# Kernel optimization log

Measured on AMD Instinct MI355X. Metric: run time of the kernel, lower is better.

The kernel has to match this reference:

```python
import jax, jax.numpy as jnp
import numpy as np

B, C, H, W, K = 16, 384, 48, 48, 3
PAD = K // 2


def _conv1x1(x, Wt, b):
    # torch Conv2d 1x1: out[b,o,h,w] = sum_i W[o,i]*x[b,i,h,w] + b[o]
    return jnp.einsum('oi,bihw->bohw', Wt, x) + b[None, :, None, None]


def setup_inputs() -> dict:
    key = jax.random.key(0)
    ks = jax.random.split(key, 11)
    s = 0.02  # small init scale for weights
    return {
        'x': jax.random.normal(ks[0], (B, C, H, W), jnp.float32),
        'Wq': jax.random.normal(ks[1], (C, C), jnp.float32) * s,
        'bq': jnp.zeros((C,), jnp.float32),
        'Wk': jax.random.normal(ks[2], (C, C), jnp.float32) * s,
        'bk': jnp.zeros((C,), jnp.float32),
        'Wv': jax.random.normal(ks[3], (C, C), jnp.float32) * s,
        'bv': jnp.zeros((C,), jnp.float32),
        'Wg': jax.random.normal(ks[4], (K * K, K * K), jnp.float32) * s,
        'bg': jnp.zeros((K * K,), jnp.float32),
        'Wp': jax.random.normal(ks[5], (C, C), jnp.float32) * s,
        'bp': jnp.zeros((C,), jnp.float32),
    }


def reference(x, Wq, bq, Wk, bk, Wv, bv, Wg, bg, Wp, bp):
    # v_proj
    value = _conv1x1(x, Wv, bv)  # [B,C,H,W]

    # _generate_kernels: q_proj -> adaptive avg pool to (K,K) -> linear(9->9)
    qk = _conv1x1(x, Wq, bq)
    # H,W divisible by K => adaptive pool == mean over equal blocks
    qk = qk.reshape(B, C, K, H // K, K, W // K).mean(axis=(3, 5))  # [B,C,K,K]
    qk = qk.reshape(B, C, K * K)
    kernels = jnp.einsum('bcp,qp->bcq', qk, Wg) + bg  # nn.Linear: x @ W.T + b
    kernels = kernels.reshape(B, C, K, K)

    # k = k_proj(global avg pool(x))  -> [B,C,1,1]
    emb = x.mean(axis=(2, 3))  # [B,C]
    k = jnp.einsum('oi,bi->bo', Wk, emb) + bk  # [B,C]

    # residual modification of kernels
    mean_per_kernel = kernels.mean(axis=(2, 3), keepdims=True)  # [B,C,1,1]
    factor = jax.nn.sigmoid(k)[:, :, None, None]
    kernels = kernels - factor * mean_per_kernel  # [B,C,K,K]

    # dynamic per-sample per-channel depthwise conv (cross-correlation, 'same' pad)
    xp = jnp.pad(value, ((0, 0), (0, 0), (PAD, PAD), (PAD, PAD)))
    # patches[b,c,p,h,w] = value[b,c,h+i-PAD,w+j-PAD], p = i*K+j
    patches = jnp.stack(
        [xp[:, :, i:i + H, j:j + W] for i in range(K) for j in range(K)], axis=2
    )  # [B,C,K*K,H,W]
    out = jnp.einsum('bcphw,bcp->bchw', patches, kernels.reshape(B, C, K * K))

    return _conv1x1(out, Wp, bp)
```

## Files before the change

### kernel.cpp

```cpp
#include <hip/hip_runtime.h>
#include <cstdint>
#include <cstddef>

#define B_  16
#define C_  384
#define H_  48
#define W_  48
#define HW_ 2304

typedef __bf16 bf16x8 __attribute__((ext_vector_type(8)));
typedef float  f32x4  __attribute__((ext_vector_type(4)));
typedef unsigned short u16x8 __attribute__((ext_vector_type(8)));

typedef __attribute__((address_space(3))) void       lds_void;
typedef const __attribute__((address_space(1))) void gbl_void;

__device__ __forceinline__ unsigned short f2bf(float f) {
    union { float f; unsigned int u; } v; v.f = f;
    unsigned int r = v.u + 0x7fffu + ((v.u >> 16) & 1u);
    return (unsigned short)(r >> 16);
}
__device__ __forceinline__ float bf2f(unsigned short u) {
    union { unsigned int u; float f; } v; v.u = ((unsigned int)u) << 16;
    return v.f;
}

__global__ void castw2_kernel(const float* __restrict__ wv, unsigned short* __restrict__ dv,
                              const float* __restrict__ wp, unsigned short* __restrict__ dp) {
    const int blk = blockIdx.x;
    const float* s = (blk < 144) ? wv : wp;
    unsigned short* d = (blk < 144) ? dv : dp;
    const int i = ((blk < 144 ? blk : blk - 144) * 256 + threadIdx.x) * 4;
    const float4 v = *(const float4*)&s[i];
    ushort4 o; o.x = f2bf(v.x); o.y = f2bf(v.y); o.z = f2bf(v.z); o.w = f2bf(v.w);
    *(ushort4*)&d[i] = o;
}

__global__ __launch_bounds__(256) void tcast_kernel(const float* __restrict__ x,
                                                    unsigned short* __restrict__ xT) {
    __shared__ unsigned short tile[64][68];
    const int t  = threadIdx.x;
    const int b  = blockIdx.z;
    const int p0 = blockIdx.x * 64, c0 = blockIdx.y * 64;
    const float* xb = x + ((size_t)b * C_ + c0) * HW_ + p0;

#pragma unroll
    for (int pass = 0; pass < 4; ++pass) {
        const int cr = pass * 16 + (t >> 4);
        const int pc = (t & 15) * 4;
        const float4 v = *(const float4*)&xb[(size_t)cr * HW_ + pc];
        tile[pc + 0][cr] = f2bf(v.x); tile[pc + 1][cr] = f2bf(v.y);
        tile[pc + 2][cr] = f2bf(v.z); tile[pc + 3][cr] = f2bf(v.w);
    }
    __syncthreads();
    unsigned short* xTb = xT + ((size_t)b * HW_ + p0) * C_ + c0;
#pragma unroll
    for (int pass = 0; pass < 4; ++pass) {
        const int pr = pass * 16 + (t >> 4);
        const int cc = (t & 15) * 4;
        *(ushort4*)&xTb[(size_t)pr * C_ + cc] = *(const ushort4*)&tile[pr][cc];
    }
}

__global__ __launch_bounds__(256) void poolT_kernel(const unsigned short* __restrict__ xT,
                                                    float* __restrict__ px) {
    const int r  = blockIdx.x;
    const int c0 = blockIdx.y * 64;
    const int b  = blockIdx.z;
    const int t  = threadIdx.x;
    const int wv = t >> 6;
    const int l  = t & 63;
    const int i  = l >> 3;
    const int cg = l & 7;
    const int ri = r / 3, rj = r % 3;
    const int cbase = c0 + cg * 8;

    __shared__ float s[4][64];

    float acc[8] = {};
#pragma unroll
    for (int k = 0; k < 8; ++k) {
        const int pix = wv * 64 + i + k * 8;
        const int h = ri * 16 + (pix >> 4), w = rj * 16 + (pix & 15);
        const u16x8 v = *(const u16x8*)&xT[((size_t)b * HW_ + h * W_ + w) * C_ + cbase];
#pragma unroll
        for (int e = 0; e < 8; ++e) acc[e] += bf2f(v[e]);
    }
#pragma unroll
    for (int m = 8; m <= 32; m <<= 1)
#pragma unroll
        for (int e = 0; e < 8; ++e) acc[e] += __shfl_xor(acc[e], m, 64);
    if (i == 0)
#pragma unroll
        for (int e = 0; e < 8; ++e) s[wv][cg * 8 + e] = acc[e];
    __syncthreads();
    if (t < 64) {
        const float tot = s[0][t] + s[1][t] + s[2][t] + s[3][t];
        px[((size_t)b * C_ + c0 + t) * 9 + r] = tot * (1.f / 256.f);
    }
}

__global__ void small_kernel(const float* __restrict__ px,
                             const float* __restrict__ Wq, const float* __restrict__ bq,
                             const float* __restrict__ Wk, const float* __restrict__ bk,
                             const float* __restrict__ Wg, const float* __restrict__ bg,
                             unsigned short* __restrict__ kernT) {
    const int b = blockIdx.y;
    const int o = blockIdx.x * 128 + threadIdx.x;

    __shared__ float px_l[C_ * 9];
    __shared__ float emb_l[C_];
    __shared__ float wg_l[81];
    __shared__ float bg_l[9];

    for (int idx = threadIdx.x; idx < C_ * 9; idx += 128) px_l[idx] = px[(size_t)b * C_ * 9 + idx];
    if (threadIdx.x < 81) wg_l[threadIdx.x] = Wg[threadIdx.x];
    if (threadIdx.x < 9)  bg_l[threadIdx.x] = bg[threadIdx.x];
    __syncthreads();
    for (int idx = threadIdx.x; idx < C_; idx += 128) {
        float s0 = 0.f;
#pragma unroll
        for (int p = 0; p < 9; ++p) s0 += px_l[idx * 9 + p];
        emb_l[idx] = s0 * (1.f / 9.f);
    }
    __syncthreads();

    float accq[9];
#pragma unroll
    for (int p = 0; p < 9; ++p) accq[p] = bq[o];
    float acck = bk[o];
    const float* wq_row = Wq + (size_t)o * C_;
    const float* wk_row = Wk + (size_t)o * C_;
    for (int i = 0; i < C_; ++i) {
        const float w = wq_row[i];
#pragma unroll
        for (int p = 0; p < 9; ++p) accq[p] = fmaf(w, px_l[i * 9 + p], accq[p]);
        acck = fmaf(wk_row[i], emb_l[i], acck);
    }

    float kf[9], mean = 0.f;
#pragma unroll
    for (int q = 0; q < 9; ++q) {
        float a = bg_l[q];
#pragma unroll
        for (int p = 0; p < 9; ++p) a = fmaf(accq[p], wg_l[q * 9 + p], a);
        kf[q] = a; mean += a;
    }
    mean *= (1.f / 9.f);
    const float sig = 1.f / (1.f + expf(-acck));
#pragma unroll
    for (int q = 0; q < 9; ++q)
        kernT[((size_t)b * 9 + q) * C_ + o] = f2bf(kf[q] - sig * mean);
}

template<int BIAS_COL, bool OUT_BF16, int BMAJOR>
__global__ __launch_bounds__(256) void gemm_bt(const unsigned short* __restrict__ A,
                                               const unsigned short* __restrict__ Bt,
                                               const float* __restrict__ bias,
                                               void* __restrict__ Yv,
                                               int N, int nMt, int nNt, int perB,
                                               long long sA, long long sB, long long sY) {
    const int q8  = gridDim.x >> 3;
    const int swz = (blockIdx.x & 7) * q8 + (blockIdx.x >> 3);
    const int b   = swz / perB;
    const int r   = swz % perB;
    const int mtile = BMAJOR ? (r % nMt) : (r / nNt);
    const int ntile = BMAJOR ? (r / nMt) : (r % nNt);
    const int m0 = mtile * 128, n0 = ntile * 128;

    const int t = threadIdx.x;
    const int l = t & 63, w = t >> 6;
    const unsigned short* Ab = A + (size_t)b * sA;
    const unsigned short* Bb = Bt + (size_t)b * sB;

    __shared__ __align__(16) unsigned short As[128 * 64];
    __shared__ __align__(16) unsigned short Bs[128 * 64];

    f32x4 acc[4][4] = {};
    const int wm = w >> 1, wn = w & 1;

    const int srow = t >> 3;
    const int skc  = t & 7;
    const int gkc  = skc ^ (srow & 7);

    const int lr = l & 15;
    const int kq = l >> 4;
    const int xorv = lr & 7;

    for (int k0 = 0; k0 < 384; k0 += 64) {
#pragma unroll
        for (int j = 0; j < 4; ++j)
            __builtin_amdgcn_global_load_lds(
                (gbl_void*)(Ab + (size_t)(m0 + 32 * j + srow) * 384 + k0 + gkc * 8),
                (lds_void*)(As + (32 * j + srow) * 64 + skc * 8), 16, 0, 0);
#pragma unroll
        for (int j = 0; j < 4; ++j)
            __builtin_amdgcn_global_load_lds(
                (gbl_void*)(Bb + (size_t)(n0 + 32 * j + srow) * 384 + k0 + gkc * 8),
                (lds_void*)(Bs + (32 * j + srow) * 64 + skc * 8), 16, 0, 0);
        __syncthreads();

#pragma unroll
        for (int sub = 0; sub < 2; ++sub) {
            const int kc = sub * 4 + kq;
            const int ko = (kc ^ xorv) * 8;
            bf16x8 af[4], bfr[4];
#pragma unroll
            for (int f = 0; f < 4; ++f)
                af[f] = *reinterpret_cast<const bf16x8*>(&As[(wm * 64 + f * 16 + lr) * 64 + ko]);
#pragma unroll
            for (int f = 0; f < 4; ++f)
                bfr[f] = *reinterpret_cast<const bf16x8*>(&Bs[(wn * 64 + f * 16 + lr) * 64 + ko]);
#pragma unroll
            for (int fm = 0; fm < 4; ++fm)
#pragma unroll
                for (int fn = 0; fn < 4; ++fn)
                    acc[fm][fn] = __builtin_amdgcn_mfma_f32_16x16x32_bf16(af[fm], bfr[fn], acc[fm][fn], 0, 0, 0);
        }
        __syncthreads();
    }

    const int lg = (l >> 4) * 4;
#pragma unroll
    for (int fm = 0; fm < 4; ++fm) {
        const int row = m0 + wm * 64 + fm * 16 + lg;
#pragma unroll
        for (int fn = 0; fn < 4; ++fn) {
            const int col = n0 + wn * 64 + fn * 16 + lr;
            const float cb = BIAS_COL ? bias[col] : 0.f;
#pragma unroll
            for (int rr = 0; rr < 4; ++rr) {
                const float v = acc[fm][fn][rr] + (BIAS_COL ? cb : bias[row + rr]);
                if (OUT_BF16)
                    ((unsigned short*)Yv)[(size_t)b * sY + (size_t)(row + rr) * N + col] = f2bf(v);
                else
                    ((float*)Yv)[(size_t)b * sY + (size_t)(row + rr) * N + col] = v;
            }
        }
    }
}

__global__ __launch_bounds__(256) void dwT_kernel(const unsigned short* __restrict__ vT,
                                                  const unsigned short* __restrict__ kT,
                                                  unsigned short* __restrict__ oT) {
    int u = blockIdx.x * 256 + threadIdx.x;
    const int cg = u % 48;  u /= 48;
    const int p  = u % HW_;
    const int b  = u / HW_;
    const int h = p / W_, w = p % W_;
    const int c0 = cg * 8;
    const size_t base = (size_t)b * HW_ * C_;

    u16x8 kv[9];
#pragma unroll
    for (int q = 0; q < 9; ++q)
        kv[q] = *(const u16x8*)&kT[((size_t)b * 9 + q) * C_ + c0];

    float acc[8] = {};
#pragma unroll
    for (int di = 0; di < 3; ++di) {
        const int hh = h + di - 1;
        if (hh < 0 || hh >= H_) continue;
#pragma unroll
        for (int dj = 0; dj < 3; ++dj) {
            const int wn = w + dj - 1;
            if (wn < 0 || wn >= W_) continue;
            const u16x8 v = *(const u16x8*)&vT[base + (size_t)(hh * W_ + wn) * C_ + c0];
            const int q = di * 3 + dj;
#pragma unroll
            for (int e = 0; e < 8; ++e)
                acc[e] = fmaf(bf2f(v[e]), bf2f(kv[q][e]), acc[e]);
        }
    }
    u16x8 o;
#pragma unroll
    for (int e = 0; e < 8; ++e) o[e] = f2bf(acc[e]);
    *(u16x8*)&oT[base + (size_t)p * C_ + c0] = o;
}

extern "C" void kernel_launch(void* const* d_in, const int* in_sizes, int n_in,
                              void* d_out, int out_size, void* d_ws, size_t ws_size,
                              hipStream_t stream) {
    const float* x  = (const float*)d_in[0];
    const float* Wq = (const float*)d_in[1];
    const float* bq = (const float*)d_in[2];
    const float* Wk = (const float*)d_in[3];
    const float* bk = (const float*)d_in[4];
    const float* Wv = (const float*)d_in[5];
    const float* bv = (const float*)d_in[6];
    const float* Wg = (const float*)d_in[7];
    const float* bg = (const float*)d_in[8];
    const float* Wp = (const float*)d_in[9];
    const float* bp = (const float*)d_in[10];
    float* out = (float*)d_out;

    char* ws = (char*)d_ws;
    const size_t bhwc2 = (size_t)B_ * HW_ * C_ * 2;
    unsigned short* xT     = (unsigned short*)ws;
    unsigned short* valueT = (unsigned short*)(ws + bhwc2);
    unsigned short* Wvb    = (unsigned short*)(ws + 2 * bhwc2);
    unsigned short* Wpb    = (unsigned short*)(ws + 2 * bhwc2 + 294912);
    float*          px     = (float*)(ws + 2 * bhwc2 + 2 * 294912);
    unsigned short* kernT  = (unsigned short*)(ws + 2 * bhwc2 + 2 * 294912 + 221184);
    unsigned short* out2T  = xT;

    castw2_kernel<<<288, 256, 0, stream>>>(Wv, Wvb, Wp, Wpb);
    tcast_kernel<<<dim3(HW_ / 64, C_ / 64, B_), 256, 0, stream>>>(x, xT);
    poolT_kernel<<<dim3(9, C_ / 64, B_), 256, 0, stream>>>(xT, px);
    small_kernel<<<dim3(3, B_), 128, 0, stream>>>(px, Wq, bq, Wk, bk, Wg, bg, kernT);

    gemm_bt<1, true, 0><<<864, 256, 0, stream>>>(
        xT, Wvb, bv, (void*)valueT, C_, 288, 3, 864, 0LL, 0LL, 0LL);

    dwT_kernel<<<dim3((B_ * HW_ * (C_ / 8)) / 256), 256, 0, stream>>>(valueT, kernT, out2T);

    gemm_bt<0, false, 1><<<864, 256, 0, stream>>>(
        Wpb, out2T, bp, (void*)out, HW_, 3, 18, 54,
        0LL, (long long)HW_ * C_, (long long)C_ * HW_);
}
```

Baseline: 125.5 us.

## Double-buffer GEMM LDS tiles with BK=32 and 2D grid for depthwise kernel

The GEMM main loop now uses two LDS buffers of 128x32 tiles and prefetches the next K slice while running MFMAs on the current one. This removes one barrier per iteration and hides global-to-LDS latency. It adds a new XOR swizzle for the 32-wide rows and raises MFMA wave priority during compute. The depthwise kernel moves the batch index into blockIdx.y, which removes an integer divide and modulo per thread.

Measured after the change: 132.6 us. 1.06x slower.

```diff
diff --git a/kernel.cpp b/kernel.cpp
--- a/kernel.cpp
+++ b/kernel.cpp
@@ -173,52 +173,73 @@
     const unsigned short* Ab = A + (size_t)b * sA;
     const unsigned short* Bb = Bt + (size_t)b * sB;
 
-    __shared__ __align__(16) unsigned short As[128 * 64];
-    __shared__ __align__(16) unsigned short Bs[128 * 64];
+    __shared__ __align__(16) unsigned short As[2][128 * 32];
+    __shared__ __align__(16) unsigned short Bs[2][128 * 32];
 
     f32x4 acc[4][4] = {};
     const int wm = w >> 1, wn = w & 1;
 
-    const int srow = t >> 3;
-    const int skc  = t & 7;
-    const int gkc  = skc ^ (srow & 7);
+    const int srow0 = t >> 2;
+    const int sc    = t & 3;
 
     const int lr = l & 15;
     const int kq = l >> 4;
-    const int xorv = lr & 7;
-
-    for (int k0 = 0; k0 < 384; k0 += 64) {
-#pragma unroll
-        for (int j = 0; j < 4; ++j)
-            __builtin_amdgcn_global_load_lds(
-                (gbl_void*)(Ab + (size_t)(m0 + 32 * j + srow) * 384 + k0 + gkc * 8),
-                (lds_void*)(As + (32 * j + srow) * 64 + skc * 8), 16, 0, 0);
-#pragma unroll
-        for (int j = 0; j < 4; ++j)
-            __builtin_amdgcn_global_load_lds(
-                (gbl_void*)(Bb + (size_t)(n0 + 32 * j + srow) * 384 + k0 + gkc * 8),
-                (lds_void*)(Bs + (32 * j + srow) * 64 + skc * 8), 16, 0, 0);
+
+#define STAGE(BUF, K0)                                                          \
+    {                                                                           \
+        _Pragma("unroll")                                                       \
+        for (int j = 0; j < 2; ++j) {                                           \
+            const int rw = 64 * j + srow0;                                      \
+            const int gk = (sc ^ ((rw >> 1) & 3)) * 8;                          \
+            __builtin_amdgcn_global_load_lds(                                   \
+                (gbl_void*)(Ab + (size_t)(m0 + rw) * 384 + (K0) + gk),          \
+                (lds_void*)(&As[BUF][0] + rw * 32 + sc * 8), 16, 0, 0);         \
+        }                                                                       \
+        _Pragma("unroll")                                                       \
+        for (int j = 0; j < 2; ++j) {                                           \
+            const int rw = 64 * j + srow0;                                      \
+            const int gk = (sc ^ ((rw >> 1) & 3)) * 8;                          \
+            __builtin_amdgcn_global_load_lds(                                   \
+                (gbl_void*)(Bb + (size_t)(n0 + rw) * 384 + (K0) + gk),          \
+                (lds_void*)(&Bs[BUF][0] + rw * 32 + sc * 8), 16, 0, 0);         \
+        }                                                                       \
+    }
+
+    STAGE(0, 0);
+    __syncthreads();
+
+    int cur = 0;
+#pragma unroll 1
+    for (int step = 0; step < 12; ++step) {
+        if (step < 11) STAGE(cur ^ 1, (step + 1) * 32);
+
+        const unsigned short* Ac = &As[cur][0];
+        const unsigned short* Bc = &Bs[cur][0];
+        bf16x8 af[4], bfr[4];
+#pragma unroll
+        for (int f = 0; f < 4; ++f) {
+            const int row = wm * 64 + f * 16 + lr;
+            const int ko  = (kq ^ ((row >> 1) & 3)) * 8;
+            af[f] = *reinterpret_cast<const bf16x8*>(&Ac[row * 32 + ko]);
+        }
+#pragma unroll
+        for (int f = 0; f < 4; ++f) {
+            const int row = wn * 64 + f * 16 + lr;
+            const int ko  = (kq ^ ((row >> 1) & 3)) * 8;
+            bfr[f] = *reinterpret_cast<const bf16x8*>(&Bc[row * 32 + ko]);
+        }
+        __builtin_amdgcn_s_setprio(1);
+#pragma unroll
+        for (int fm = 0; fm < 4; ++fm)
+#pragma unroll
+            for (int fn = 0; fn < 4; ++fn)
+                acc[fm][fn] = __builtin_amdgcn_mfma_f32_16x16x32_bf16(af[fm], bfr[fn], acc[fm][fn], 0, 0, 0);
+        __builtin_amdgcn_s_setprio(0);
+
         __syncthreads();
-
-#pragma unroll
-        for (int sub = 0; sub < 2; ++sub) {
-            const int kc = sub * 4 + kq;
-            const int ko = (kc ^ xorv) * 8;
-            bf16x8 af[4], bfr[4];
-#pragma unroll
-            for (int f = 0; f < 4; ++f)
-                af[f] = *reinterpret_cast<const bf16x8*>(&As[(wm * 64 + f * 16 + lr) * 64 + ko]);
-#pragma unroll
-            for (int f = 0; f < 4; ++f)
-                bfr[f] = *reinterpret_cast<const bf16x8*>(&Bs[(wn * 64 + f * 16 + lr) * 64 + ko]);
-#pragma unroll
-            for (int fm = 0; fm < 4; ++fm)
-#pragma unroll
-                for (int fn = 0; fn < 4; ++fn)
-                    acc[fm][fn] = __builtin_amdgcn_mfma_f32_16x16x32_bf16(af[fm], bfr[fn], acc[fm][fn], 0, 0, 0);
-        }
-        __syncthreads();
-    }
+        cur ^= 1;
+    }
+#undef STAGE
 
     const int lg = (l >> 4) * 4;
 #pragma unroll
@@ -243,10 +264,10 @@
 __global__ __launch_bounds__(256) void dwT_kernel(const unsigned short* __restrict__ vT,
                                                   const unsigned short* __restrict__ kT,
                                                   unsigned short* __restrict__ oT) {
+    const int b = blockIdx.y;
     int u = blockIdx.x * 256 + threadIdx.x;
-    const int cg = u % 48;  u /= 48;
-    const int p  = u % HW_;
-    const int b  = u / HW_;
+    const int cg = u % 48;
+    const int p  = u / 48;
     const int h = p / W_, w = p % W_;
     const int c0 = cg * 8;
     const size_t base = (size_t)b * HW_ * C_;
@@ -312,7 +333,7 @@
     gemm_bt<1, true, 0><<<864, 256, 0, stream>>>(
         xT, Wvb, bv, (void*)valueT, C_, 288, 3, 864, 0LL, 0LL, 0LL);
 
-    dwT_kernel<<<dim3((B_ * HW_ * (C_ / 8)) / 256), 256, 0, stream>>>(valueT, kernT, out2T);
+    dwT_kernel<<<dim3(432, B_), 256, 0, stream>>>(valueT, kernT, out2T);
 
     gemm_bt<0, false, 1><<<864, 256, 0, stream>>>(
         Wpb, out2T, bp, (void*)out, HW_, 3, 18, 54,
```

## Merge weight cast into transpose kernel and give depthwise threads four pixels

Applied to the files above, without the earlier changes.

Folds the Wv/Wp bf16 cast into the x transpose-cast kernel as extra blocks, removing one launch. Reworks the depthwise 3x3 kernel so each thread computes four horizontally adjacent pixels from a 3x6 register window of loaded rows. Each input vector is then reused across output pixels, which cuts redundant global loads and per-thread kernel-weight loads. In exchange, each thread holds more registers and the grid has fewer threads.

After: 116.3 us. 1.08x faster.

```diff
diff --git a/kernel.cpp b/kernel.cpp
--- a/kernel.cpp
+++ b/kernel.cpp
@@ -25,40 +25,47 @@
     return v.f;
 }
 
-__global__ void castw2_kernel(const float* __restrict__ wv, unsigned short* __restrict__ dv,
-                              const float* __restrict__ wp, unsigned short* __restrict__ dp) {
+__global__ __launch_bounds__(256) void tcastw_kernel(const float* __restrict__ x,
+                                                     const float* __restrict__ Wv,
+                                                     const float* __restrict__ Wp,
+                                                     unsigned short* __restrict__ Wvb,
+                                                     unsigned short* __restrict__ Wpb,
+                                                     unsigned short* __restrict__ xT) {
+    __shared__ unsigned short tile[64][68];
     const int blk = blockIdx.x;
-    const float* s = (blk < 144) ? wv : wp;
-    unsigned short* d = (blk < 144) ? dv : dp;
-    const int i = ((blk < 144 ? blk : blk - 144) * 256 + threadIdx.x) * 4;
-    const float4 v = *(const float4*)&s[i];
-    ushort4 o; o.x = f2bf(v.x); o.y = f2bf(v.y); o.z = f2bf(v.z); o.w = f2bf(v.w);
-    *(ushort4*)&d[i] = o;
-}
-
-__global__ __launch_bounds__(256) void tcast_kernel(const float* __restrict__ x,
-                                                    unsigned short* __restrict__ xT) {
-    __shared__ unsigned short tile[64][68];
-    const int t  = threadIdx.x;
-    const int b  = blockIdx.z;
-    const int p0 = blockIdx.x * 64, c0 = blockIdx.y * 64;
-    const float* xb = x + ((size_t)b * C_ + c0) * HW_ + p0;
-
-#pragma unroll
-    for (int pass = 0; pass < 4; ++pass) {
-        const int cr = pass * 16 + (t >> 4);
-        const int pc = (t & 15) * 4;
-        const float4 v = *(const float4*)&xb[(size_t)cr * HW_ + pc];
-        tile[pc + 0][cr] = f2bf(v.x); tile[pc + 1][cr] = f2bf(v.y);
-        tile[pc + 2][cr] = f2bf(v.z); tile[pc + 3][cr] = f2bf(v.w);
-    }
-    __syncthreads();
-    unsigned short* xTb = xT + ((size_t)b * HW_ + p0) * C_ + c0;
-#pragma unroll
-    for (int pass = 0; pass < 4; ++pass) {
-        const int pr = pass * 16 + (t >> 4);
-        const int cc = (t & 15) * 4;
-        *(ushort4*)&xTb[(size_t)pr * C_ + cc] = *(const ushort4*)&tile[pr][cc];
+    const int t   = threadIdx.x;
+
+    if (blk < 3456) {
+        const int b    = blk / 216;
+        const int r216 = blk % 216;
+        const int c0   = (r216 / 36) * 64;
+        const int p0   = (r216 % 36) * 64;
+        const float* xb = x + ((size_t)b * C_ + c0) * HW_ + p0;
+
+#pragma unroll
+        for (int pass = 0; pass < 4; ++pass) {
+            const int cr = pass * 16 + (t >> 4);
+            const int pc = (t & 15) * 4;
+            const float4 v = *(const float4*)&xb[(size_t)cr * HW_ + pc];
+            tile[pc + 0][cr] = f2bf(v.x); tile[pc + 1][cr] = f2bf(v.y);
+            tile[pc + 2][cr] = f2bf(v.z); tile[pc + 3][cr] = f2bf(v.w);
+        }
+        __syncthreads();
+        unsigned short* xTb = xT + ((size_t)b * HW_ + p0) * C_ + c0;
+#pragma unroll
+        for (int pass = 0; pass < 4; ++pass) {
+            const int pr = pass * 16 + (t >> 4);
+            const int cc = (t & 15) * 4;
+            *(ushort4*)&xTb[(size_t)pr * C_ + cc] = *(const ushort4*)&tile[pr][cc];
+        }
+    } else {
+        const int cblk = blk - 3456;
+        const float* s = (cblk < 144) ? Wv : Wp;
+        unsigned short* d = (cblk < 144) ? Wvb : Wpb;
+        const int i = ((cblk < 144 ? cblk : cblk - 144) * 256 + t) * 4;
+        const float4 v = *(const float4*)&s[i];
+        ushort4 o; o.x = f2bf(v.x); o.y = f2bf(v.y); o.z = f2bf(v.z); o.w = f2bf(v.w);
+        *(ushort4*)&d[i] = o;
     }
 }
 
@@ -243,11 +250,13 @@
 __global__ __launch_bounds__(256) void dwT_kernel(const unsigned short* __restrict__ vT,
                                                   const unsigned short* __restrict__ kT,
                                                   unsigned short* __restrict__ oT) {
-    int u = blockIdx.x * 256 + threadIdx.x;
-    const int cg = u % 48;  u /= 48;
-    const int p  = u % HW_;
-    const int b  = u / HW_;
-    const int h = p / W_, w = p % W_;
+    const int b = blockIdx.y;
+    const int u = blockIdx.x * 256 + threadIdx.x;
+    const int cg = u % 48;
+    const int pg = u / 48;
+    const int p0 = pg * 4;
+    const int h  = p0 / W_;
+    const int w0 = p0 % W_;
     const int c0 = cg * 8;
     const size_t base = (size_t)b * HW_ * C_;
 
@@ -256,26 +265,39 @@
     for (int q = 0; q < 9; ++q)
         kv[q] = *(const u16x8*)&kT[((size_t)b * 9 + q) * C_ + c0];
 
-    float acc[8] = {};
+    const u16x8 zero = {};
+    u16x8 v[3][6];
 #pragma unroll
     for (int di = 0; di < 3; ++di) {
         const int hh = h + di - 1;
-        if (hh < 0 || hh >= H_) continue;
-#pragma unroll
-        for (int dj = 0; dj < 3; ++dj) {
-            const int wn = w + dj - 1;
-            if (wn < 0 || wn >= W_) continue;
-            const u16x8 v = *(const u16x8*)&vT[base + (size_t)(hh * W_ + wn) * C_ + c0];
-            const int q = di * 3 + dj;
-#pragma unroll
-            for (int e = 0; e < 8; ++e)
-                acc[e] = fmaf(bf2f(v[e]), bf2f(kv[q][e]), acc[e]);
-        }
-    }
-    u16x8 o;
-#pragma unroll
-    for (int e = 0; e < 8; ++e) o[e] = f2bf(acc[e]);
-    *(u16x8*)&oT[base + (size_t)p * C_ + c0] = o;
+        const bool hok = (hh >= 0) && (hh < H_);
+#pragma unroll
+        for (int c = 0; c < 6; ++c) {
+            const int wn = w0 + c - 1;
+            const bool ok = hok && (wn >= 0) && (wn < W_);
+            v[di][c] = ok ? *(const u16x8*)&vT[base + (size_t)(hh * W_ + wn) * C_ + c0]
+                          : zero;
+        }
+    }
+
+#pragma unroll
+    for (int j = 0; j < 4; ++j) {
+        float acc[8] = {};
+#pragma unroll
+        for (int di = 0; di < 3; ++di)
+#pragma unroll
+            for (int dj = 0; dj < 3; ++dj) {
+                const int q = di * 3 + dj;
+                const u16x8 vv = v[di][j + dj];
+#pragma unroll
+                for (int e = 0; e < 8; ++e)
+                    acc[e] = fmaf(bf2f(vv[e]), bf2f(kv[q][e]), acc[e]);
+            }
+        u16x8 o;
+#pragma unroll
+        for (int e = 0; e < 8; ++e) o[e] = f2bf(acc[e]);
+        *(u16x8*)&oT[base + (size_t)(p0 + j) * C_ + c0] = o;
+    }
 }
 
 extern "C" void kernel_launch(void* const* d_in, const int* in_sizes, int n_in,
@@ -304,16 +326,12 @@
     unsigned short* kernT  = (unsigned short*)(ws + 2 * bhwc2 + 2 * 294912 + 221184);
     unsigned short* out2T  = xT;
 
-    castw2_kernel<<<288, 256, 0, stream>>>(Wv, Wvb, Wp, Wpb);
-    tcast_kernel<<<dim3(HW_ / 64, C_ / 64, B_), 256, 0, stream>>>(x, xT);
+    tcastw_kernel<<<3744, 256, 0, stream>>>(x, Wv, Wp, Wvb, Wpb, xT);
     poolT_kernel<<<dim3(9, C_ / 64, B_), 256, 0, stream>>>(xT, px);
     small_kernel<<<dim3(3, B_), 128, 0, stream>>>(px, Wq, bq, Wk, bk, Wg, bg, kernT);
-
     gemm_bt<1, true, 0><<<864, 256, 0, stream>>>(
         xT, Wvb, bv, (void*)valueT, C_, 288, 3, 864, 0LL, 0LL, 0LL);
-
-    dwT_kernel<<<dim3((B_ * HW_ * (C_ / 8)) / 256), 256, 0, stream>>>(valueT, kernT, out2T);
-
+    dwT_kernel<<<dim3(108, B_), 256, 0, stream>>>(valueT, kernT, out2T);
     gemm_bt<0, false, 1><<<864, 256, 0, stream>>>(
         Wpb, out2T, bp, (void*)out, HW_, 3, 18, 54,
         0LL, (long long)HW_ * C_, (long long)C_ * HW_);
```
